# Performance work log

Hardware: AMD Instinct MI355X
Metric: run time of the kernel (lower is better)

Reference implementation:

```python
import jax, jax.numpy as jnp
import numpy as np

N_NODES = 50000
N_EDGES = 400000
N_GRAPHS = 128
IN_CH = 768
COND = 768
HID = 128
HEADS = 4


def _gat_conv(x, src, dst, W, att_src, att_dst, bias):
    """PyG-style GATConv (concat=True, negative_slope=0.2). x:[N,Fin], W:[Fin,H*D]."""
    N = x.shape[0]
    H, D = att_src.shape
    h = (x @ W).reshape(N, H, D)                      # [N,H,D]
    a_src = jnp.sum(h * att_src, axis=-1)             # [N,H]
    a_dst = jnp.sum(h * att_dst, axis=-1)             # [N,H]
    alpha = jax.nn.leaky_relu(a_src[src] + a_dst[dst], 0.2)   # [E,H]
    m = jax.ops.segment_max(alpha, dst, num_segments=N)       # per-dst max (stable softmax)
    alpha = jnp.exp(alpha - m[dst])
    s = jax.ops.segment_sum(alpha, dst, num_segments=N)
    alpha = alpha / (s[dst] + 1e-16)                  # PyG softmax eps
    msg = h[src] * alpha[:, :, None]                  # [E,H,D]
    out = jax.ops.segment_sum(msg, dst, num_segments=N)       # [N,H,D]
    return out.reshape(N, H * D) + bias


def setup_inputs() -> dict:
    key = jax.random.key(0)
    ks = jax.random.split(key, 12)

    def glorot(k, shape):
        fan = shape[0] + shape[-1]
        return jax.random.normal(k, shape, jnp.float32) * jnp.sqrt(2.0 / fan)

    x = jax.random.normal(ks[0], (N_NODES, IN_CH), jnp.float32)
    substring_embed = jax.random.normal(ks[1], (N_GRAPHS, COND), jnp.float32)
    edge_index = jax.random.randint(ks[2], (2, N_EDGES), 0, N_NODES)
    batch = jnp.sort(jax.random.randint(ks[3], (N_NODES,), 0, N_GRAPHS))

    W1 = glorot(ks[4], (IN_CH + COND, HEADS * HID))
    att_src1 = glorot(ks[5], (HEADS, HID))
    att_dst1 = glorot(ks[6], (HEADS, HID))
    b1 = jnp.zeros((HEADS * HID,), jnp.float32)

    W2 = glorot(ks[7], (HEADS * HID, 1 * HID))
    att_src2 = glorot(ks[8], (1, HID))
    att_dst2 = glorot(ks[9], (1, HID))
    b2 = jnp.zeros((HID,), jnp.float32)

    out_W = glorot(ks[10], (HID, 1))
    out_b = jnp.zeros((1,), jnp.float32)

    return {"x": x, "substring_embed": substring_embed,
            "W1": W1, "att_src1": att_src1, "att_dst1": att_dst1, "b1": b1,
            "W2": W2, "att_src2": att_src2, "att_dst2": att_dst2, "b2": b2,
            "out_W": out_W, "out_b": out_b,
            "edge_index": edge_index, "batch": batch}


def reference(x, substring_embed, W1, att_src1, att_dst1, b1,
              W2, att_src2, att_dst2, b2, out_W, out_b,
              edge_index, batch):
    N = x.shape[0]
    loops = jnp.arange(N)                              # PyG add_self_loops=True
    src = jnp.concatenate([edge_index[0], loops])
    dst = jnp.concatenate([edge_index[1], loops])

    h = jnp.concatenate([x, substring_embed[batch]], axis=-1)   # [N, IN+COND]
    h = jax.nn.relu(_gat_conv(h, src, dst, W1, att_src1, att_dst1, b1))
    h = jax.nn.relu(_gat_conv(h, src, dst, W2, att_src2, att_dst2, b2))
    out = (h @ out_W + out_b)[:, 0]                    # squeeze(-1) -> [N]
    return out
```

## Files before the change

kernel.cpp:

```cpp
#include <hip/hip_runtime.h>
#include <hip/hip_bf16.h>
#include <cstdint>
#include <cstddef>

#define NN 50000
#define NE 400000
#define ET (NE + NN)
#define NG 128
#define INCH 768
#define CONDCH 768
#define HIDD 128
#define NHEAD 4
#define F1 (NHEAD * HIDD)
#define F2 HIDD
#define MPAD 50176

typedef unsigned short ushort_t;
typedef float f32x4 __attribute__((ext_vector_type(4)));
typedef __bf16 bf16x8 __attribute__((ext_vector_type(8)));

typedef const void __attribute__((address_space(1))) as1_void;
typedef void __attribute__((address_space(3))) as3_void;

__device__ __forceinline__ void gload_lds16(const void* g, void* l) {
    __builtin_amdgcn_global_load_lds((as1_void*)g, (as3_void*)l, 16, 0, 0);
}

__device__ __forceinline__ ushort_t f2bf(float f) {
    uint32_t u = __float_as_uint(f);
    uint32_t r = (u + 0x7fffu + ((u >> 16) & 1u)) >> 16;
    return (ushort_t)r;
}
__device__ __forceinline__ float bf_lo(uint32_t u) { return __uint_as_float(u << 16); }
__device__ __forceinline__ float bf_hi(uint32_t u) { return __uint_as_float(u & 0xffff0000u); }

__global__ __launch_bounds__(256) void k_cvt(const float* __restrict__ in,
                                             ushort_t* __restrict__ out, long n4,
                                             int* __restrict__ deg) {
    long i = (long)blockIdx.x * blockDim.x + threadIdx.x;
    if (deg && i < NN) deg[i] = 1;
    if (i >= n4) return;
    float4 v = *(const float4*)(in + i * 4);
    ushort4 o;
    o.x = f2bf(v.x); o.y = f2bf(v.y); o.z = f2bf(v.z); o.w = f2bf(v.w);
    *(ushort4*)(out + i * 4) = o;
}

#define R1 (F1 * INCH)
#define R2 (R1 + F1 * CONDCH)
#define R3 (R2 + F2 * F1)
__global__ __launch_bounds__(256) void k_tcvt_all(
    const float* __restrict__ W1, const float* __restrict__ W2,
    ushort_t* __restrict__ W1aT, ushort_t* __restrict__ W1cT, ushort_t* __restrict__ W2T)
{
    int idx = blockIdx.x * blockDim.x + threadIdx.x;
    if (idx >= R3) return;
    if (idx < R1) {
        int n = idx / INCH, k = idx % INCH;
        W1aT[idx] = f2bf(W1[(size_t)k * F1 + n]);
    } else if (idx < R2) {
        int j = idx - R1;
        int n = j / CONDCH, k = j % CONDCH;
        W1cT[j] = f2bf(W1[(size_t)(INCH + k) * F1 + n]);
    } else {
        int j = idx - R2;
        int n = j / F1, k = j % F1;
        W2T[j] = f2bf(W2[(size_t)k * F2 + n]);
    }
}

template <int TM, bool ADD_GATHER, bool OUT_BF16, bool FUSE_ATT>
__global__ __launch_bounds__(TM * 2) void k_mgemm(
    const ushort_t* __restrict__ A, const ushort_t* __restrict__ BT, void* __restrict__ Cv,
    int M, int N, int K, int nBN,
    const float* __restrict__ G, const int* __restrict__ gidx,
    const float* __restrict__ attS, const float* __restrict__ attD,
    float* __restrict__ aS, float* __restrict__ aD, int attStride)
{
    __shared__ __align__(16) char smem[TM * 64 + 8192];
    char* sA = smem;
    char* sB = smem + TM * 64;

    const int nwg = gridDim.x;
    const int orig = blockIdx.x;
    const int q = nwg >> 3, r = nwg & 7;
    const int xcd = orig & 7, sid = orig >> 3;
    const int wg = (xcd < r ? xcd * (q + 1) : r * (q + 1) + (xcd - r) * q) + sid;
    const int bx = wg / nBN, by = wg % nBN;

    const int tid = threadIdx.x;
    const int lane = tid & 63;
    const int wave = tid >> 6;
    const int wr = wave >> 1, wc = wave & 1;
    const int m0 = bx * TM, n0 = by * 128;

    const int sr = tid >> 2;
    const int sc = (tid & 3) * 8;
    const ushort_t* gA = A + (size_t)(m0 + sr) * K + sc;
    const ushort_t* gB = BT + (size_t)(n0 + sr) * K + sc;
    const int ldsw = wave * 1024;

    const int a_off = (wr * 64 + (lane & 15)) * 64 + (lane >> 4) * 16;
    const int b_off = (wc * 64 + (lane & 15)) * 64 + (lane >> 4) * 16;

    f32x4 acc[4][4];
#pragma unroll
    for (int i = 0; i < 4; i++)
#pragma unroll
        for (int j = 0; j < 4; j++) acc[i][j] = 0.f;

    for (int kt = 0; kt < K; kt += 32) {
        gload_lds16(gA + kt,                         sA + ldsw);
        gload_lds16(gA + (size_t)(TM / 2) * K + kt,  sA + TM * 32 + ldsw);
        gload_lds16(gB + kt,                         sB + ldsw);
        if (TM == 128)
            gload_lds16(gB + (size_t)64 * K + kt,    sB + 4096 + ldsw);
        __syncthreads();
        bf16x8 af[4], bfr[4];
#pragma unroll
        for (int i = 0; i < 4; i++) af[i]  = *(const bf16x8*)(sA + a_off + i * 1024);
#pragma unroll
        for (int j = 0; j < 4; j++) bfr[j] = *(const bf16x8*)(sB + b_off + j * 1024);
#pragma unroll
        for (int i = 0; i < 4; i++)
#pragma unroll
            for (int j = 0; j < 4; j++)
                acc[i][j] = __builtin_amdgcn_mfma_f32_16x16x32_bf16(af[i], bfr[j], acc[i][j], 0, 0, 0);
        __syncthreads();
    }

    float asv[4], adv[4];
    if (FUSE_ATT) {
#pragma unroll
        for (int j = 0; j < 4; j++) {
            int col = wc * 64 + j * 16 + (lane & 15);
            asv[j] = attS[by * 128 + col];
            adv[j] = attD[by * 128 + col];
        }
    }
    float* redS = (float*)smem;
    float* redD = (float*)smem + 2 * TM;

#pragma unroll
    for (int i = 0; i < 4; i++) {
        int mbase = m0 + wr * 64 + i * 16 + (lane >> 4) * 4;
#pragma unroll
        for (int rr = 0; rr < 4; rr++) {
            int m = mbase + rr;
            if (m >= M) continue;
            const float* grow = nullptr;
            if (ADD_GATHER) grow = G + (size_t)gidx[m] * N;
            float vs = 0.f, vd = 0.f;
#pragma unroll
            for (int j = 0; j < 4; j++) {
                int n = n0 + wc * 64 + j * 16 + (lane & 15);
                float v = acc[i][j][rr];
                if (ADD_GATHER) v += grow[n];
                if (OUT_BF16) ((ushort_t*)Cv)[(size_t)m * N + n] = f2bf(v);
                else          ((float*)Cv)[(size_t)m * N + n] = v;
                if (FUSE_ATT) { vs = fmaf(v, asv[j], vs); vd = fmaf(v, adv[j], vd); }
            }
            if (FUSE_ATT) {
#pragma unroll
                for (int o = 1; o < 16; o <<= 1) { vs += __shfl_xor(vs, o); vd += __shfl_xor(vd, o); }
                if ((lane & 15) == 0) {
                    int mloc = wr * 64 + i * 16 + (lane >> 4) * 4 + rr;
                    redS[wc * TM + mloc] = vs;
                    redD[wc * TM + mloc] = vd;
                }
            }
        }
    }
    if (FUSE_ATT) {
        __syncthreads();
        int sd = tid >= TM ? 1 : 0, mloc = tid & (TM - 1);
        int m = m0 + mloc;
        if (m < M) {
            const float* rb = sd ? redD : redS;
            float v = rb[mloc] + rb[TM + mloc];
            (sd ? aD : aS)[(size_t)m * attStride + by] = v;
        }
    }
}

__global__ void k_deg(const int* __restrict__ ei, int* __restrict__ deg)
{
    int e = blockIdx.x * blockDim.x + threadIdx.x;
    if (e >= NE) return;
    atomicAdd(&deg[ei[NE + e]], 1);
}

#define SCB 196
__global__ __launch_bounds__(256) void k_deg_bsum(const int* __restrict__ deg, int* __restrict__ bsum) {
    int i = blockIdx.x * 256 + threadIdx.x;
    int v = (i < NN) ? deg[i] : 0;
    for (int o = 32; o; o >>= 1) v += __shfl_xor(v, o);
    __shared__ int wsum[4];
    if ((threadIdx.x & 63) == 0) wsum[threadIdx.x >> 6] = v;
    __syncthreads();
    if (threadIdx.x == 0) bsum[blockIdx.x] = wsum[0] + wsum[1] + wsum[2] + wsum[3];
}
__global__ __launch_bounds__(256) void k_bsum_scan(int* __restrict__ bsum, int* __restrict__ bbase,
                                                  int* __restrict__ row_ptr) {
    int t = threadIdx.x;
    int v = (t < SCB) ? bsum[t] : 0;
    int x = v;
    for (int o = 1; o < 64; o <<= 1) { int y = __shfl_up(x, o); if ((t & 63) >= o) x += y; }
    __shared__ int wsum[4];
    if ((t & 63) == 63) wsum[t >> 6] = x;
    __syncthreads();
    int base = 0;
    for (int w = 0; w < (t >> 6); w++) base += wsum[w];
    if (t < SCB) bbase[t] = base + x - v;
    if (t == 0) row_ptr[NN] = wsum[0] + wsum[1] + wsum[2] + wsum[3];
}
__global__ __launch_bounds__(256) void k_scan_final(const int* __restrict__ deg, const int* __restrict__ bbase,
                                                    int* __restrict__ row_ptr, int* __restrict__ cursor) {
    int b = blockIdx.x;
    int t = threadIdx.x;
    int i = b * 256 + t;
    int v = (i < NN) ? deg[i] : 0;
    int x = v;
    for (int o = 1; o < 64; o <<= 1) { int y = __shfl_up(x, o); if ((t & 63) >= o) x += y; }
    __shared__ int wsum[4];
    if ((t & 63) == 63) wsum[t >> 6] = x;
    __syncthreads();
    int base = bbase[b];
    for (int w = 0; w < (t >> 6); w++) base += wsum[w];
    int excl = base + x - v;
    if (i < NN) { row_ptr[i] = excl; cursor[i] = excl; }
}

__global__ void k_scatter(const int* __restrict__ ei, int* __restrict__ cursor,
                          int* __restrict__ csr_src)
{
    int e = blockIdx.x * blockDim.x + threadIdx.x;
    if (e >= ET) return;
    int src = e < NE ? ei[e] : e - NE;
    int dst = e < NE ? ei[NE + e] : e - NE;
    int pos = atomicAdd(&cursor[dst], 1);
    csr_src[pos] = src;
}

__global__ __launch_bounds__(256) void k_agg1(
    const ushort_t* __restrict__ h1, const float* __restrict__ a_src, const float* __restrict__ a_dst,
    const int* __restrict__ row_ptr, const int* __restrict__ csr_src,
    const float* __restrict__ b1, ushort_t* __restrict__ g1)
{
    const int n = blockIdx.x * 4 + (threadIdx.x >> 6);
    const int lane = threadIdx.x & 63;
    const int head = lane >> 4;
    const int beg = row_ptr[n], end = row_ptr[n + 1];
    const float4 ad = *(const float4*)(a_dst + (size_t)n * 4);

    float mx[4] = {-1e30f, -1e30f, -1e30f, -1e30f};
    for (int p = beg + lane; p < end; p += 64) {
        int src = csr_src[p];
        float4 as = *(const float4*)(a_src + (size_t)src * 4);
        float v;
        v = as.x + ad.x; v = v >= 0.f ? v : 0.2f * v; mx[0] = fmaxf(mx[0], v);
        v = as.y + ad.y; v = v >= 0.f ? v : 0.2f * v; mx[1] = fmaxf(mx[1], v);
        v = as.z + ad.z; v = v >= 0.f ? v : 0.2f * v; mx[2] = fmaxf(mx[2], v);
        v = as.w + ad.w; v = v >= 0.f ? v : 0.2f * v; mx[3] = fmaxf(mx[3], v);
    }
#pragma unroll
    for (int o = 32; o; o >>= 1) {
        mx[0] = fmaxf(mx[0], __shfl_xor(mx[0], o));
        mx[1] = fmaxf(mx[1], __shfl_xor(mx[1], o));
        mx[2] = fmaxf(mx[2], __shfl_xor(mx[2], o));
        mx[3] = fmaxf(mx[3], __shfl_xor(mx[3], o));
    }
    const float m   = (head & 1) ? ((head & 2) ? mx[3] : mx[1]) : ((head & 2) ? mx[2] : mx[0]);
    const float adh = (head & 1) ? ((head & 2) ? ad.w : ad.y)   : ((head & 2) ? ad.z : ad.x);

    float ssum = 0.f;
    float a[8] = {0.f, 0.f, 0.f, 0.f, 0.f, 0.f, 0.f, 0.f};
    int p = beg;
#define LREL(l) ((l) >= 0.f ? (l) : 0.2f * (l))
#define ACC8(c, u) \
        a[0] = fmaf(c, bf_lo(u.x), a[0]); a[1] = fmaf(c, bf_hi(u.x), a[1]); \
        a[2] = fmaf(c, bf_lo(u.y), a[2]); a[3] = fmaf(c, bf_hi(u.y), a[3]); \
        a[4] = fmaf(c, bf_lo(u.z), a[4]); a[5] = fmaf(c, bf_hi(u.z), a[5]); \
        a[6] = fmaf(c, bf_lo(u.w), a[6]); a[7] = fmaf(c, bf_hi(u.w), a[7]);
    for (; p + 3 < end; p += 4) {
        int s0 = csr_src[p], s1 = csr_src[p + 1], s2 = csr_src[p + 2], s3 = csr_src[p + 3];
        uint4 u0 = *(const uint4*)(h1 + (size_t)s0 * F1 + lane * 8);
        uint4 u1 = *(const uint4*)(h1 + (size_t)s1 * F1 + lane * 8);
        uint4 u2 = *(const uint4*)(h1 + (size_t)s2 * F1 + lane * 8);
        uint4 u3 = *(const uint4*)(h1 + (size_t)s3 * F1 + lane * 8);
        float c0 = expf(LREL(a_src[s0 * 4 + head] + adh) - m);
        float c1 = expf(LREL(a_src[s1 * 4 + head] + adh) - m);
        float c2 = expf(LREL(a_src[s2 * 4 + head] + adh) - m);
        float c3 = expf(LREL(a_src[s3 * 4 + head] + adh) - m);
        ssum += c0 + c1 + c2 + c3;
        ACC8(c0, u0) ACC8(c1, u1) ACC8(c2, u2) ACC8(c3, u3)
    }
    for (; p < end; p++) {
        int s0 = csr_src[p];
        uint4 u0 = *(const uint4*)(h1 + (size_t)s0 * F1 + lane * 8);
        float c0 = expf(LREL(a_src[s0 * 4 + head] + adh) - m);
        ssum += c0;
        ACC8(c0, u0)
    }
#undef ACC8
    const float inv = 1.0f / (ssum + 1e-16f);
    const int ch = lane * 8;
    float4 bA = *(const float4*)(b1 + ch);
    float4 bB = *(const float4*)(b1 + ch + 4);
    uint4 ov;
    ov.x = (uint32_t)f2bf(fmaxf(fmaf(a[0], inv, bA.x), 0.f)) | ((uint32_t)f2bf(fmaxf(fmaf(a[1], inv, bA.y), 0.f)) << 16);
    ov.y = (uint32_t)f2bf(fmaxf(fmaf(a[2], inv, bA.z), 0.f)) | ((uint32_t)f2bf(fmaxf(fmaf(a[3], inv, bA.w), 0.f)) << 16);
    ov.z = (uint32_t)f2bf(fmaxf(fmaf(a[4], inv, bB.x), 0.f)) | ((uint32_t)f2bf(fmaxf(fmaf(a[5], inv, bB.y), 0.f)) << 16);
    ov.w = (uint32_t)f2bf(fmaxf(fmaf(a[6], inv, bB.z), 0.f)) | ((uint32_t)f2bf(fmaxf(fmaf(a[7], inv, bB.w), 0.f)) << 16);
    *(uint4*)(g1 + (size_t)n * F1 + ch) = ov;
}

__global__ __launch_bounds__(256) void k_agg2(
    const ushort_t* __restrict__ h2, const float* __restrict__ a_src, const float* __restrict__ a_dst,
    const int* __restrict__ row_ptr, const int* __restrict__ csr_src,
    const float* __restrict__ b2, const float* __restrict__ outW, const float* __restrict__ outb,
    float* __restrict__ out)
{
    const int n = blockIdx.x * 4 + (threadIdx.x >> 6);
    const int lane = threadIdx.x & 63;
    const int beg = row_ptr[n], end = row_ptr[n + 1];
    const float ad = a_dst[n];

    float mx = -1e30f;
    for (int p = beg + lane; p < end; p += 64) {
        float v = a_src[csr_src[p]] + ad;
        v = v >= 0.f ? v : 0.2f * v;
        mx = fmaxf(mx, v);
    }
#pragma unroll
    for (int o = 32; o; o >>= 1) mx = fmaxf(mx, __shfl_xor(mx, o));

    float ssum = 0.f;
    float a0 = 0.f, a1 = 0.f;
    int p = beg;
    for (; p + 3 < end; p += 4) {
        int s0 = csr_src[p], s1 = csr_src[p + 1], s2 = csr_src[p + 2], s3 = csr_src[p + 3];
        uint32_t u0 = *(const uint32_t*)(h2 + (size_t)s0 * F2 + lane * 2);
        uint32_t u1 = *(const uint32_t*)(h2 + (size_t)s1 * F2 + lane * 2);
        uint32_t u2 = *(const uint32_t*)(h2 + (size_t)s2 * F2 + lane * 2);
        uint32_t u3 = *(const uint32_t*)(h2 + (size_t)s3 * F2 + lane * 2);
        float c0 = expf(LREL(a_src[s0] + ad) - mx);
        float c1 = expf(LREL(a_src[s1] + ad) - mx);
        float c2 = expf(LREL(a_src[s2] + ad) - mx);
        float c3 = expf(LREL(a_src[s3] + ad) - mx);
        ssum += c0 + c1 + c2 + c3;
        a0 = fmaf(c0, bf_lo(u0), a0); a1 = fmaf(c0, bf_hi(u0), a1);
        a0 = fmaf(c1, bf_lo(u1), a0); a1 = fmaf(c1, bf_hi(u1), a1);
        a0 = fmaf(c2, bf_lo(u2), a0); a1 = fmaf(c2, bf_hi(u2), a1);
        a0 = fmaf(c3, bf_lo(u3), a0); a1 = fmaf(c3, bf_hi(u3), a1);
    }
    for (; p < end; p++) {
        int s0 = csr_src[p];
        uint32_t u0 = *(const uint32_t*)(h2 + (size_t)s0 * F2 + lane * 2);
        float c0 = expf(LREL(a_src[s0] + ad) - mx);
        ssum += c0;
        a0 = fmaf(c0, bf_lo(u0), a0); a1 = fmaf(c0, bf_hi(u0), a1);
    }
    const float inv = 1.0f / (ssum + 1e-16f);
    float v0 = fmaf(a0, inv, b2[lane * 2]);     v0 = v0 > 0.f ? v0 : 0.f;
    float v1 = fmaf(a1, inv, b2[lane * 2 + 1]); v1 = v1 > 0.f ? v1 : 0.f;
    float pr = v0 * outW[lane * 2] + v1 * outW[lane * 2 + 1];
    for (int o = 32; o; o >>= 1) pr += __shfl_xor(pr, o);
    if (lane == 0) out[n] = pr + outb[0];
}

extern "C" void kernel_launch(void* const* d_in, const int* in_sizes, int n_in,
                              void* d_out, int out_size, void* d_ws, size_t ws_size,
                              hipStream_t stream)
{
    const float* x        = (const float*)d_in[0];
    const float* cond     = (const float*)d_in[1];
    const float* W1       = (const float*)d_in[2];
    const float* att_src1 = (const float*)d_in[3];
    const float* att_dst1 = (const float*)d_in[4];
    const float* b1       = (const float*)d_in[5];
    const float* W2       = (const float*)d_in[6];
    const float* att_src2 = (const float*)d_in[7];
    const float* att_dst2 = (const float*)d_in[8];
    const float* b2       = (const float*)d_in[9];
    const float* outW     = (const float*)d_in[10];
    const float* outb     = (const float*)d_in[11];
    const int*   ei       = (const int*)d_in[12];
    const int*   batch    = (const int*)d_in[13];
    float* out = (float*)d_out;

    char* ws = (char*)d_ws;
    size_t off = 0;
    auto alloc = [&](size_t bytes) { void* p = ws + off; off += (bytes + 255) & ~size_t(255); return p; };
    ushort_t* xb      = (ushort_t*)alloc((size_t)MPAD * INCH * 2);
    ushort_t* condb   = (ushort_t*)alloc((size_t)NG * CONDCH * 2);
    ushort_t* W1aT    = (ushort_t*)alloc((size_t)F1 * INCH * 2);
    ushort_t* W1cT    = (ushort_t*)alloc((size_t)F1 * CONDCH * 2);
    ushort_t* W2T     = (ushort_t*)alloc((size_t)F2 * F1 * 2);
    float*    C2      = (float*)alloc((size_t)NG * F1 * 4);
    ushort_t* h1b     = (ushort_t*)alloc((size_t)NN * F1 * 2);
    float*    a_src1  = (float*)alloc((size_t)NN * NHEAD * 4);
    float*    a_dst1  = (float*)alloc((size_t)NN * NHEAD * 4);
    int*      deg     = (int*)alloc((size_t)NN * 4);
    int*      cursor  = (int*)alloc((size_t)NN * 4);
    int*      row_ptr = (int*)alloc((size_t)(NN + 1) * 4);
    int*      csr_src = (int*)alloc((size_t)ET * 4);
    int*      bsum    = (int*)alloc((size_t)SCB * 4);
    int*      bbase   = (int*)alloc((size_t)SCB * 4);
    ushort_t* h2b     = (ushort_t*)alloc((size_t)NN * F2 * 2);
    float*    a_src2  = (float*)alloc((size_t)NN * 4);
    float*    a_dst2  = (float*)alloc((size_t)NN * 4);
    ushort_t* g1b     = xb;
    (void)ws_size;

    {
        long n4 = (long)NN * INCH / 4;
        k_cvt<<<(int)((n4 + 255) / 256), 256, 0, stream>>>(x, xb, n4, deg);
        n4 = (long)NG * CONDCH / 4;
        k_cvt<<<(int)((n4 + 255) / 256), 256, 0, stream>>>(cond, condb, n4, nullptr);
        k_tcvt_all<<<(R3 + 255) / 256, 256, 0, stream>>>(W1, W2, W1aT, W1cT, W2T);
    }

    k_deg<<<(NE + 255) / 256, 256, 0, stream>>>(ei, deg);
    k_deg_bsum<<<SCB, 256, 0, stream>>>(deg, bsum);
    k_bsum_scan<<<1, 256, 0, stream>>>(bsum, bbase, row_ptr);
    k_scan_final<<<SCB, 256, 0, stream>>>(deg, bbase, row_ptr, cursor);
    k_scatter<<<(ET + 255) / 256, 256, 0, stream>>>(ei, cursor, csr_src);

    k_mgemm<128, false, false, false><<<4, 256, 0, stream>>>(
        condb, W1cT, C2, NG, F1, CONDCH, 4,
        nullptr, nullptr, nullptr, nullptr, nullptr, nullptr, 0);
    k_mgemm<256, true, true, true><<<(MPAD / 256) * 4, 512, 0, stream>>>(
        xb, W1aT, h1b, NN, F1, INCH, 4,
        C2, batch, att_src1, att_dst1, a_src1, a_dst1, NHEAD);
    k_agg1<<<NN / 4, 256, 0, stream>>>(h1b, a_src1, a_dst1, row_ptr, csr_src, b1, g1b);
    k_mgemm<256, false, true, true><<<MPAD / 256, 512, 0, stream>>>(
        g1b, W2T, h2b, NN, F2, F1, 1,
        nullptr, nullptr, att_src2, att_dst2, a_src2, a_dst2, 1);
    k_agg2<<<NN / 4, 256, 0, stream>>>(h2b, a_src2, a_dst2, row_ptr, csr_src, b2, outW, outb, out);
}
```

Baseline: 326.7 us.

## Double-buffer GEMM LDS tiles to overlap global loads with MFMA

Turns the k-loop of the bf16 MFMA GEMM into a two-stage pipeline. The next K tile is loaded into a second LDS buffer while the current tile is multiplied, and vmcnt waits plus raw barriers replace the full syncthreads. This aims to hide global-to-LDS load latency behind compute, at the cost of twice the LDS per block, which can lower occupancy. The hand-counted vmcnt values must match the number of loads each stage issues per TM.

```diff
diff --git a/kernel.cpp b/kernel.cpp
--- a/kernel.cpp
+++ b/kernel.cpp
@@ -77,9 +77,11 @@
     const float* __restrict__ attS, const float* __restrict__ attD,
     float* __restrict__ aS, float* __restrict__ aD, int attStride)
 {
-    __shared__ __align__(16) char smem[TM * 64 + 8192];
+    constexpr int SA = TM * 64;
+    constexpr int SB = 8192;
+    __shared__ __align__(16) char smem[2 * SA + 2 * SB];
     char* sA = smem;
-    char* sB = smem + TM * 64;
+    char* sB = smem + 2 * SA;
 
     const int nwg = gridDim.x;
     const int orig = blockIdx.x;
@@ -103,30 +105,47 @@
     const int a_off = (wr * 64 + (lane & 15)) * 64 + (lane >> 4) * 16;
     const int b_off = (wc * 64 + (lane & 15)) * 64 + (lane >> 4) * 16;
 
+    auto STAGE = [&](int kt, int b) {
+        char* dA = sA + b * SA + ldsw;
+        gload_lds16(gA + kt, dA);
+        gload_lds16(gA + (size_t)(TM / 2) * K + kt, dA + SA / 2);
+        char* dB = sB + b * SB + ldsw;
+        gload_lds16(gB + kt, dB);
+        if (TM == 128)
+            gload_lds16(gB + (size_t)64 * K + kt, dB + 4096);
+    };
+
     f32x4 acc[4][4];
 #pragma unroll
     for (int i = 0; i < 4; i++)
 #pragma unroll
         for (int j = 0; j < 4; j++) acc[i][j] = 0.f;
 
-    for (int kt = 0; kt < K; kt += 32) {
-        gload_lds16(gA + kt,                         sA + ldsw);
-        gload_lds16(gA + (size_t)(TM / 2) * K + kt,  sA + TM * 32 + ldsw);
-        gload_lds16(gB + kt,                         sB + ldsw);
-        if (TM == 128)
-            gload_lds16(gB + (size_t)64 * K + kt,    sB + 4096 + ldsw);
-        __syncthreads();
+    STAGE(0, 0);
+    const int nt = K / 32;
+    for (int t = 0; t < nt; t++) {
+        const int cur = t & 1;
+        if (t + 1 < nt) {
+            STAGE((t + 1) * 32, cur ^ 1);
+            if constexpr (TM == 256) { asm volatile("s_waitcnt vmcnt(3)" ::: "memory"); }
+            else                     { asm volatile("s_waitcnt vmcnt(4)" ::: "memory"); }
+        } else {
+            asm volatile("s_waitcnt vmcnt(0)" ::: "memory");
+        }
+        __builtin_amdgcn_s_barrier();
+        __builtin_amdgcn_sched_barrier(0);
         bf16x8 af[4], bfr[4];
 #pragma unroll
-        for (int i = 0; i < 4; i++) af[i]  = *(const bf16x8*)(sA + a_off + i * 1024);
-#pragma unroll
-        for (int j = 0; j < 4; j++) bfr[j] = *(const bf16x8*)(sB + b_off + j * 1024);
+        for (int i = 0; i < 4; i++) af[i]  = *(const bf16x8*)(sA + cur * SA + a_off + i * 1024);
+#pragma unroll
+        for (int j = 0; j < 4; j++) bfr[j] = *(const bf16x8*)(sB + cur * SB + b_off + j * 1024);
 #pragma unroll
         for (int i = 0; i < 4; i++)
 #pragma unroll
             for (int j = 0; j < 4; j++)
                 acc[i][j] = __builtin_amdgcn_mfma_f32_16x16x32_bf16(af[i], bfr[j], acc[i][j], 0, 0, 0);
-        __syncthreads();
+        __builtin_amdgcn_sched_barrier(0);
+        __builtin_amdgcn_s_barrier();
     }
 
     float asv[4], adv[4];
```

Result: faster. 312.3 us (-4.4%).
